# Performance work log

Hardware: AMD Instinct MI355X
Metric: run time of the kernel (lower is better)

## Reference

```python
import jax, jax.numpy as jnp
import numpy as np

B, N, M, D = 1, 16384, 16384, 3
CHUNK = 2048          # x tile size for the online-min KNN pass
NN_WEIGHT = 1.0       # self.nn_weight
# both_ways=False, free_weight=0, ch_normals_K=0 -> only cham_x branch is active


def setup_inputs() -> dict:
    key = jax.random.key(0)
    k1, k2, k3 = jax.random.split(key, 3)
    # LiDAR-like point clouds, scaled to a ~20 m scene extent
    pc1 = jax.random.normal(k1, (B, N, D), dtype=jnp.float32) * 10.0
    est_flow = jax.random.normal(k2, (B, N, D), dtype=jnp.float32) * 0.1
    pc2 = jax.random.normal(k3, (B, M, D), dtype=jnp.float32) * 10.0
    return {"pc1": pc1, "est_flow": est_flow, "pc2": pc2}


def _knn1_l1_dists(x, y):
    """Per-point min L1 distance from x [N,3] to y [M,3], tiled over x.

    Equivalent to knn_points(x, y, K=1, norm=1).dists[..., 0] without
    materializing the full [N, M] distance matrix.
    """
    n = x.shape[0]
    x_tiles = x.reshape(n // CHUNK, CHUNK, D)

    def tile_min(xc):  # xc: [CHUNK, 3]
        d = jnp.sum(jnp.abs(xc[:, None, :] - y[None, :, :]), axis=-1)  # [CHUNK, M]
        return jnp.min(d, axis=-1)                                     # [CHUNK]

    return jax.lax.map(tile_min, x_tiles).reshape(n)


def reference(pc1, est_flow, pc2):
    x = pc1 + est_flow                                   # deformed cloud [B,N,3]
    cham_x = jax.vmap(_knn1_l1_dists)(x, pc2)            # [B, N]
    cham_y = jnp.float32(0.0)                            # both_ways=False
    freespace_loss = jnp.zeros_like(cham_x)              # free_weight == 0 branch
    chamf_loss = NN_WEIGHT * (cham_x.mean() + cham_y)    # free_weight * 0 omitted
    return (chamf_loss, freespace_loss)
```

## Files before the change

### kernel.cpp

```cpp
#include <hip/hip_runtime.h>


#define TPB 256
#define RB 2
#define PTS_PER_BLOCK (TPB * RB)
#define MAX_MSEG 512

__global__ __launch_bounds__(TPB) void init_min_kernel(unsigned* __restrict__ minbits, int N) {
    int i = blockIdx.x * TPB + threadIdx.x;
    if (i < N) minbits[i] = 0x7F800000u;
}

__global__ __launch_bounds__(TPB) void chamfer_partial_kernel(
    const float* __restrict__ pc1, const float* __restrict__ flow,
    const float* __restrict__ pc2, unsigned* __restrict__ minbits,
    int N, int M, int mseg) {
    __shared__ float4 ys[MAX_MSEG];

    const int t  = threadIdx.x;
    const int y0 = blockIdx.y * mseg;
    const int len = (M - y0 < mseg) ? (M - y0) : mseg;

    for (int j = t; j < len; j += TPB) {
        const int g = y0 + j;
        ys[j] = make_float4(pc2[3 * g], pc2[3 * g + 1], pc2[3 * g + 2], 0.0f);
    }

    const int i0 = blockIdx.x * PTS_PER_BLOCK + t;
    const int i1 = i0 + TPB;
    const bool v0 = (i0 < N), v1 = (i1 < N);

    float a0 = 0.f, a1 = 0.f, a2 = 0.f, b0 = 0.f, b1 = 0.f, b2 = 0.f;
    if (v0) {
        a0 = pc1[3 * i0]     + flow[3 * i0];
        a1 = pc1[3 * i0 + 1] + flow[3 * i0 + 1];
        a2 = pc1[3 * i0 + 2] + flow[3 * i0 + 2];
    }
    if (v1) {
        b0 = pc1[3 * i1]     + flow[3 * i1];
        b1 = pc1[3 * i1 + 1] + flow[3 * i1 + 1];
        b2 = pc1[3 * i1 + 2] + flow[3 * i1 + 2];
    }
    __syncthreads();

    float mA0 = 1e30f, mA1 = 1e30f, mB0 = 1e30f, mB1 = 1e30f;
    int j = 0;
#pragma unroll 4
    for (; j + 1 < len; j += 2) {
        const float4 ya = ys[j];
        const float4 yb = ys[j + 1];
        mA0 = fminf(mA0, fabsf(a0 - ya.x) + fabsf(a1 - ya.y) + fabsf(a2 - ya.z));
        mB0 = fminf(mB0, fabsf(b0 - ya.x) + fabsf(b1 - ya.y) + fabsf(b2 - ya.z));
        mA1 = fminf(mA1, fabsf(a0 - yb.x) + fabsf(a1 - yb.y) + fabsf(a2 - yb.z));
        mB1 = fminf(mB1, fabsf(b0 - yb.x) + fabsf(b1 - yb.y) + fabsf(b2 - yb.z));
    }
    if (j < len) {
        const float4 ya = ys[j];
        mA0 = fminf(mA0, fabsf(a0 - ya.x) + fabsf(a1 - ya.y) + fabsf(a2 - ya.z));
        mB0 = fminf(mB0, fabsf(b0 - ya.x) + fabsf(b1 - ya.y) + fabsf(b2 - ya.z));
    }
    const float mA = fminf(mA0, mA1);
    const float mB = fminf(mB0, mB1);

    if (v0) atomicMin(&minbits[i0], __float_as_uint(mA));
    if (v1) atomicMin(&minbits[i1], __float_as_uint(mB));
}

__global__ __launch_bounds__(TPB) void sum_partial_kernel(
    const unsigned* __restrict__ minbits, float* __restrict__ partials, int N) {
    int i = blockIdx.x * TPB + threadIdx.x;
    float v = (i < N) ? __uint_as_float(minbits[i]) : 0.0f;
#pragma unroll
    for (int off = 32; off > 0; off >>= 1) v += __shfl_down(v, off, 64);
    __shared__ float ls[TPB / 64];
    const int wid = threadIdx.x >> 6, lane = threadIdx.x & 63;
    if (lane == 0) ls[wid] = v;
    __syncthreads();
    if (threadIdx.x == 0) {
        float s = 0.0f;
        for (int w = 0; w < TPB / 64; ++w) s += ls[w];
        partials[blockIdx.x] = s;
    }
}

__global__ void final_kernel(const float* __restrict__ partials, int nPart,
                             float* __restrict__ out, float invN) {
    float v = 0.0f;
    for (int i = threadIdx.x; i < nPart; i += 64) v += partials[i];
#pragma unroll
    for (int off = 32; off > 0; off >>= 1) v += __shfl_down(v, off, 64);
    if (threadIdx.x == 0) out[0] = v * invN;
}

extern "C" void kernel_launch(void* const* d_in, const int* in_sizes, int n_in,
                              void* d_out, int out_size, void* d_ws, size_t ws_size,
                              hipStream_t stream) {
    const float* pc1  = (const float*)d_in[0];
    const float* flow = (const float*)d_in[1];
    const float* pc2  = (const float*)d_in[2];
    float* out = (float*)d_out;

    const int N = in_sizes[0] / 3;
    const int M = in_sizes[2] / 3;

    unsigned* minbits = (unsigned*)d_ws;
    float* partials = (float*)((char*)d_ws + (size_t)N * sizeof(unsigned));

    hipMemsetAsync(d_out, 0, (size_t)out_size * sizeof(float), stream);

    const int nbN    = (N + PTS_PER_BLOCK - 1) / PTS_PER_BLOCK;
    const int msplit = (M + MAX_MSEG - 1) / MAX_MSEG;
    const int mseg   = (M + msplit - 1) / msplit;
    const int nPart  = (N + TPB - 1) / TPB;

    init_min_kernel<<<(N + TPB - 1) / TPB, TPB, 0, stream>>>(minbits, N);
    chamfer_partial_kernel<<<dim3(nbN, msplit), TPB, 0, stream>>>(pc1, flow, pc2, minbits, N, M, mseg);
    sum_partial_kernel<<<nPart, TPB, 0, stream>>>(minbits, partials, N);
    final_kernel<<<1, 64, 0, stream>>>(partials, nPart, out, 1.0f / (float)N);
}
```

Before: 50.06 us.

## Read pc2 from global via uniform loads, raise points per thread, merge reductions

The chamfer kernel no longer stages pc2 into shared memory. Every thread reads the y points straight from global memory, where the addresses are uniform across the block and should become scalar loads. Register blocking goes from 2 to 4 x points per thread, and the M segment shrinks to 256, which gives 16x64 blocks. The init kernel is replaced by a memset to 0x7F7F7F7F, a huge finite float that still works as the atomicMin sentinel, and the two reduction kernels become one 1024-thread kernel. This cuts the launch count and the LDS traffic, at the cost of a single-block final reduction and more atomics per point.

Result: no change. 51.06 us (+2.0%).

```diff
diff --git a/kernel.cpp b/kernel.cpp
--- a/kernel.cpp
+++ b/kernel.cpp
@@ -2,94 +2,88 @@
 
 
 #define TPB 256
-#define RB 2
+#define RB 4
 #define PTS_PER_BLOCK (TPB * RB)
-#define MAX_MSEG 512
+#define MSEG 256
 
-__global__ __launch_bounds__(TPB) void init_min_kernel(unsigned* __restrict__ minbits, int N) {
-    int i = blockIdx.x * TPB + threadIdx.x;
-    if (i < N) minbits[i] = 0x7F800000u;
-}
-
-__global__ __launch_bounds__(TPB) void chamfer_partial_kernel(
+__global__ __launch_bounds__(TPB) void chamfer_kernel(
     const float* __restrict__ pc1, const float* __restrict__ flow,
     const float* __restrict__ pc2, unsigned* __restrict__ minbits,
-    int N, int M, int mseg) {
-    __shared__ float4 ys[MAX_MSEG];
+    int N, int M) {
+    const int t = threadIdx.x;
+    const int ibase = blockIdx.x * PTS_PER_BLOCK + t;
 
-    const int t  = threadIdx.x;
-    const int y0 = blockIdx.y * mseg;
-    const int len = (M - y0 < mseg) ? (M - y0) : mseg;
-
-    for (int j = t; j < len; j += TPB) {
-        const int g = y0 + j;
-        ys[j] = make_float4(pc2[3 * g], pc2[3 * g + 1], pc2[3 * g + 2], 0.0f);
+    float ax[RB], ay[RB], az[RB];
+    bool valid[RB];
+#pragma unroll
+    for (int r = 0; r < RB; ++r) {
+        int i = ibase + r * TPB;
+        valid[r] = (i < N);
+        int ic = valid[r] ? i : (N - 1);
+        ax[r] = pc1[3 * ic]     + flow[3 * ic];
+        ay[r] = pc1[3 * ic + 1] + flow[3 * ic + 1];
+        az[r] = pc1[3 * ic + 2] + flow[3 * ic + 2];
     }
 
-    const int i0 = blockIdx.x * PTS_PER_BLOCK + t;
-    const int i1 = i0 + TPB;
-    const bool v0 = (i0 < N), v1 = (i1 < N);
+    const int y0 = blockIdx.y * MSEG;
+    const int len = (M - y0 < MSEG) ? (M - y0) : MSEG;
+    const float* __restrict__ ys = pc2 + (size_t)3 * (size_t)y0;
 
-    float a0 = 0.f, a1 = 0.f, a2 = 0.f, b0 = 0.f, b1 = 0.f, b2 = 0.f;
-    if (v0) {
-        a0 = pc1[3 * i0]     + flow[3 * i0];
-        a1 = pc1[3 * i0 + 1] + flow[3 * i0 + 1];
-        a2 = pc1[3 * i0 + 2] + flow[3 * i0 + 2];
+    float m[RB];
+#pragma unroll
+    for (int r = 0; r < RB; ++r) m[r] = 3.0e38f;
+
+    if (len == MSEG) {
+#pragma unroll 4
+        for (int j = 0; j < MSEG; j += 2) {
+            const float y0x = ys[3 * j + 0], y0y = ys[3 * j + 1], y0z = ys[3 * j + 2];
+            const float y1x = ys[3 * j + 3], y1y = ys[3 * j + 4], y1z = ys[3 * j + 5];
+#pragma unroll
+            for (int r = 0; r < RB; ++r) {
+                const float d0 = fabsf(ax[r] - y0x) + fabsf(ay[r] - y0y) + fabsf(az[r] - y0z);
+                const float d1 = fabsf(ax[r] - y1x) + fabsf(ay[r] - y1y) + fabsf(az[r] - y1z);
+                m[r] = fminf(fminf(m[r], d0), d1);
+            }
+        }
+    } else {
+        for (int j = 0; j < len; ++j) {
+            const float yx = ys[3 * j + 0], yy = ys[3 * j + 1], yz = ys[3 * j + 2];
+#pragma unroll
+            for (int r = 0; r < RB; ++r) {
+                const float d = fabsf(ax[r] - yx) + fabsf(ay[r] - yy) + fabsf(az[r] - yz);
+                m[r] = fminf(m[r], d);
+            }
+        }
     }
-    if (v1) {
-        b0 = pc1[3 * i1]     + flow[3 * i1];
-        b1 = pc1[3 * i1 + 1] + flow[3 * i1 + 1];
-        b2 = pc1[3 * i1 + 2] + flow[3 * i1 + 2];
-    }
-    __syncthreads();
 
-    float mA0 = 1e30f, mA1 = 1e30f, mB0 = 1e30f, mB1 = 1e30f;
-    int j = 0;
-#pragma unroll 4
-    for (; j + 1 < len; j += 2) {
-        const float4 ya = ys[j];
-        const float4 yb = ys[j + 1];
-        mA0 = fminf(mA0, fabsf(a0 - ya.x) + fabsf(a1 - ya.y) + fabsf(a2 - ya.z));
-        mB0 = fminf(mB0, fabsf(b0 - ya.x) + fabsf(b1 - ya.y) + fabsf(b2 - ya.z));
-        mA1 = fminf(mA1, fabsf(a0 - yb.x) + fabsf(a1 - yb.y) + fabsf(a2 - yb.z));
-        mB1 = fminf(mB1, fabsf(b0 - yb.x) + fabsf(b1 - yb.y) + fabsf(b2 - yb.z));
-    }
-    if (j < len) {
-        const float4 ya = ys[j];
-        mA0 = fminf(mA0, fabsf(a0 - ya.x) + fabsf(a1 - ya.y) + fabsf(a2 - ya.z));
-        mB0 = fminf(mB0, fabsf(b0 - ya.x) + fabsf(b1 - ya.y) + fabsf(b2 - ya.z));
-    }
-    const float mA = fminf(mA0, mA1);
-    const float mB = fminf(mB0, mB1);
-
-    if (v0) atomicMin(&minbits[i0], __float_as_uint(mA));
-    if (v1) atomicMin(&minbits[i1], __float_as_uint(mB));
-}
-
-__global__ __launch_bounds__(TPB) void sum_partial_kernel(
-    const unsigned* __restrict__ minbits, float* __restrict__ partials, int N) {
-    int i = blockIdx.x * TPB + threadIdx.x;
-    float v = (i < N) ? __uint_as_float(minbits[i]) : 0.0f;
 #pragma unroll
-    for (int off = 32; off > 0; off >>= 1) v += __shfl_down(v, off, 64);
-    __shared__ float ls[TPB / 64];
-    const int wid = threadIdx.x >> 6, lane = threadIdx.x & 63;
-    if (lane == 0) ls[wid] = v;
-    __syncthreads();
-    if (threadIdx.x == 0) {
-        float s = 0.0f;
-        for (int w = 0; w < TPB / 64; ++w) s += ls[w];
-        partials[blockIdx.x] = s;
+    for (int r = 0; r < RB; ++r) {
+        if (valid[r]) atomicMin(&minbits[ibase + r * TPB], __float_as_uint(m[r]));
     }
 }
 
-__global__ void final_kernel(const float* __restrict__ partials, int nPart,
-                             float* __restrict__ out, float invN) {
-    float v = 0.0f;
-    for (int i = threadIdx.x; i < nPart; i += 64) v += partials[i];
+__global__ __launch_bounds__(1024) void reduce_kernel(
+    const unsigned* __restrict__ minbits, float* __restrict__ out, int N) {
+    float s = 0.0f;
+    const uint4* p = (const uint4*)minbits;
+    for (int k = threadIdx.x; k < N / 4; k += 1024) {
+        uint4 v = p[k];
+        s += __uint_as_float(v.x) + __uint_as_float(v.y) +
+             __uint_as_float(v.z) + __uint_as_float(v.w);
+    }
+    for (int k = (N / 4) * 4 + threadIdx.x; k < N; k += 1024)
+        s += __uint_as_float(minbits[k]);
 #pragma unroll
-    for (int off = 32; off > 0; off >>= 1) v += __shfl_down(v, off, 64);
-    if (threadIdx.x == 0) out[0] = v * invN;
+    for (int off = 32; off > 0; off >>= 1) s += __shfl_down(s, off, 64);
+    __shared__ float ls[16];
+    const int wid = threadIdx.x >> 6, lane = threadIdx.x & 63;
+    if (lane == 0) ls[wid] = s;
+    __syncthreads();
+    if (threadIdx.x == 0) {
+        float tot = 0.0f;
+        for (int w = 0; w < 16; ++w) tot += ls[w];
+        out[0] = tot / (float)N;
+    }
 }
 
 extern "C" void kernel_launch(void* const* d_in, const int* in_sizes, int n_in,
@@ -104,17 +98,13 @@
     const int M = in_sizes[2] / 3;
 
     unsigned* minbits = (unsigned*)d_ws;
-    float* partials = (float*)((char*)d_ws + (size_t)N * sizeof(unsigned));
 
     hipMemsetAsync(d_out, 0, (size_t)out_size * sizeof(float), stream);
+    hipMemsetAsync(minbits, 0x7F, (size_t)N * sizeof(unsigned), stream);
 
     const int nbN    = (N + PTS_PER_BLOCK - 1) / PTS_PER_BLOCK;
-    const int msplit = (M + MAX_MSEG - 1) / MAX_MSEG;
-    const int mseg   = (M + msplit - 1) / msplit;
-    const int nPart  = (N + TPB - 1) / TPB;
+    const int msplit = (M + MSEG - 1) / MSEG;
 
-    init_min_kernel<<<(N + TPB - 1) / TPB, TPB, 0, stream>>>(minbits, N);
-    chamfer_partial_kernel<<<dim3(nbN, msplit), TPB, 0, stream>>>(pc1, flow, pc2, minbits, N, M, mseg);
-    sum_partial_kernel<<<nPart, TPB, 0, stream>>>(minbits, partials, N);
-    final_kernel<<<1, 64, 0, stream>>>(partials, nPart, out, 1.0f / (float)N);
+    chamfer_kernel<<<dim3(nbN, msplit), TPB, 0, stream>>>(pc1, flow, pc2, minbits, N, M);
+    reduce_kernel<<<1, 1024, 0, stream>>>(minbits, out, N);
 }
```
